# Performance work log

Hardware: AMD Instinct MI355X
Metric: run time of the kernel (lower is better)

## Reference

```python
import jax, jax.numpy as jnp
import numpy as np

DIM = 1024
HEADS = 16
DIM_HEAD = 64
INNER = HEADS * DIM_HEAD
EPS = 1e-5

def layernorm(x, g, b):
    mu = jnp.mean(x, axis=-1, keepdims=True)
    var = jnp.var(x, axis=-1, keepdims=True)
    return (x - mu) * jax.lax.rsqrt(var + EPS) * g + b

def setup_inputs() -> dict:
    key = jax.random.key(0)
    ks = jax.random.split(key, 9)
    b, t, n, m = 8, 8, 576, 64
    x = jax.random.normal(ks[0], (b, t, n, DIM), dtype=jnp.float32)
    latents = jax.random.normal(ks[1], (b, t, m, DIM), dtype=jnp.float32)
    att_mask = jax.random.randint(ks[2], (b, t, n), 0, 2, dtype=jnp.int32)
    s = 1.0 / np.sqrt(DIM)
    Wq = jax.random.normal(ks[3], (DIM, INNER), dtype=jnp.float32) * s
    Wkv = jax.random.normal(ks[4], (DIM, 2 * INNER), dtype=jnp.float32) * s
    Wo = jax.random.normal(ks[5], (INNER, DIM), dtype=jnp.float32) * (1.0 / np.sqrt(INNER))
    gm = jnp.ones((DIM,), jnp.float32); bm = jnp.zeros((DIM,), jnp.float32)
    gl = jnp.ones((DIM,), jnp.float32); bl = jnp.zeros((DIM,), jnp.float32)
    return {"x": x, "latents": latents, "att_mask": att_mask,
            "gm": gm, "bm": bm, "gl": gl, "bl": bl,
            "Wq": Wq, "Wkv": Wkv, "Wo": Wo}

def reference(x, latents, att_mask, gm, bm, gl, bl, Wq, Wkv, Wo):
    b, t, n, d = x.shape
    m = latents.shape[2]
    h, dh = HEADS, DIM_HEAD
    scale = dh ** -0.5

    xn = layernorm(x, gm, bm)
    ln = layernorm(latents, gl, bl)

    q = ln @ Wq                                  # b t m inner
    kv_input = jnp.concatenate((xn, ln), axis=-2)  # b t (n+m) d
    kv = kv_input @ Wkv                          # b t (n+m) 2*inner
    k, v = jnp.split(kv, 2, axis=-1)

    # b t s (h dh) -> b h t s dh
    def split_heads(a):
        bb, tt, ss, _ = a.shape
        return a.reshape(bb, tt, ss, h, dh).transpose(0, 3, 1, 2, 4)
    q = split_heads(q) * scale
    k = split_heads(k)
    v = split_heads(v)

    sim = jnp.einsum('bhtid,bhtjd->bhtij', q, k)   # b h t m (n+m)

    # mask: concat ones for latent KV positions; broadcast over heads and query dim
    full_mask = jnp.concatenate(
        [att_mask.astype(sim.dtype), jnp.ones((b, t, m), sim.dtype)], axis=2)  # b t (n+m)
    neg = jnp.finfo(sim.dtype).min
    bias = jnp.where(full_mask > 0, 0.0, neg)      # b t (n+m)
    sim = sim + bias[:, None, :, None, :]

    attn = jax.nn.softmax(sim, axis=-1)
    out = jnp.einsum('bhtij,bhtjd->bhtid', attn, v)  # b h t m dh
    out = out.transpose(0, 2, 3, 1, 4).reshape(b, t, m, h * dh)
    return out @ Wo
```

## Files before the change

### kernel.cpp

```cpp
#include <hip/hip_runtime.h>
#include <hip/hip_bf16.h>
#include <stdint.h>

#define NCTX 576
#define MLAT 64
#define SEQ 640
#define DMODEL 1024
#define NH 16
#define DHEAD 64
#define INNER_ 1024
#define KV_W 2048

typedef float f32x4 __attribute__((ext_vector_type(4)));
typedef __bf16 bf16x8 __attribute__((ext_vector_type(8)));
typedef unsigned short u16;
typedef unsigned int u32;
typedef unsigned long long u64;

typedef __attribute__((address_space(1))) u32 as1_u32;
typedef __attribute__((address_space(3))) u32 as3_u32;

__device__ __forceinline__ u16 f2bf(float f) {
    u32 u = __builtin_bit_cast(u32, f);
    u32 r = (u + 0x7fffu + ((u >> 16) & 1u)) >> 16;
    return (u16)r;
}

__device__ __forceinline__ int xcd_swizzle(int orig, int nwg) {
    int q = nwg >> 3, r = nwg & 7;
    int xcd = orig & 7, loc = orig >> 3;
    return (xcd < r ? xcd * (q + 1) : r * (q + 1) + (xcd - r) * q) + loc;
}

__global__ __launch_bounds__(256) void transpose_cast(const float* __restrict__ src,
                                                      u16* __restrict__ dst, int K, int N) {
    __shared__ float tile[64][65];
    int k0 = blockIdx.y * 64, n0 = blockIdx.x * 64;
    int tid = threadIdx.x;
#pragma unroll
    for (int i = 0; i < 4; ++i) {
        int idx = i * 256 + tid;
        int kk = idx >> 4;
        int nn = (idx & 15) << 2;
        float4 v = *(const float4*)(src + (u64)(k0 + kk) * N + n0 + nn);
        tile[kk][nn] = v.x; tile[kk][nn + 1] = v.y; tile[kk][nn + 2] = v.z; tile[kk][nn + 3] = v.w;
    }
    __syncthreads();
#pragma unroll
    for (int i = 0; i < 4; ++i) {
        int idx = i * 256 + tid;
        int nn = idx >> 4;
        int kk = (idx & 15) << 2;
        ushort4 o;
        o.x = f2bf(tile[kk][nn]);     o.y = f2bf(tile[kk + 1][nn]);
        o.z = f2bf(tile[kk + 2][nn]); o.w = f2bf(tile[kk + 3][nn]);
        *(ushort4*)(dst + (u64)(n0 + nn) * K + k0 + kk) = o;
    }
}

__global__ __launch_bounds__(256) void ln_cast(const float* __restrict__ x,
                                               const float* __restrict__ lat,
                                               const float* __restrict__ gm, const float* __restrict__ bm,
                                               const float* __restrict__ gl, const float* __restrict__ bl,
                                               u16* __restrict__ out) {
    int row = blockIdx.x;
    int bt = row / SEQ, s = row - bt * SEQ;
    const float *src, *g, *b;
    if (s < NCTX) { src = x + ((u64)bt * NCTX + s) * DMODEL; g = gm; b = bm; }
    else          { src = lat + ((u64)bt * MLAT + (s - NCTX)) * DMODEL; g = gl; b = bl; }
    int tid = threadIdx.x;
    float4 v = *(const float4*)(src + tid * 4);
    float sum = v.x + v.y + v.z + v.w;
    float sq  = v.x * v.x + v.y * v.y + v.z * v.z + v.w * v.w;
#pragma unroll
    for (int off = 1; off < 64; off <<= 1) {
        sum += __shfl_xor(sum, off, 64);
        sq  += __shfl_xor(sq, off, 64);
    }
    __shared__ float red[8];
    int w = tid >> 6, lane = tid & 63;
    if (lane == 0) { red[w] = sum; red[4 + w] = sq; }
    __syncthreads();
    sum = red[0] + red[1] + red[2] + red[3];
    sq  = red[4] + red[5] + red[6] + red[7];
    float mu = sum * (1.0f / DMODEL);
    float var = sq * (1.0f / DMODEL) - mu * mu;
    float rstd = rsqrtf(var + 1e-5f);
    float4 gv = *(const float4*)(g + tid * 4);
    float4 bv = *(const float4*)(b + tid * 4);
    ushort4 o;
    o.x = f2bf((v.x - mu) * rstd * gv.x + bv.x);
    o.y = f2bf((v.y - mu) * rstd * gv.y + bv.y);
    o.z = f2bf((v.z - mu) * rstd * gv.z + bv.z);
    o.w = f2bf((v.w - mu) * rstd * gv.w + bv.w);
    *(ushort4*)(out + (u64)row * DMODEL + tid * 4) = o;
}

template <typename OUT_T>
__global__ __launch_bounds__(256) void gemm_bf16(const u16* __restrict__ A,
                                                 const u16* __restrict__ Bt,
                                                 OUT_T* __restrict__ C,
                                                 int M, int ldc,
                                                 int rpgL2, long long gstride, float scale) {
    constexpr int K = 1024;
    __shared__ u16 As[128 * 32];
    __shared__ u16 Bs[128 * 32];
    int tid = threadIdx.x;
    int lane = tid & 63;
    int w = tid >> 6;
    int wm = w >> 1, wn = w & 1;
    int nwg = gridDim.x * gridDim.y;
    int wg = xcd_swizzle(blockIdx.y * gridDim.x + blockIdx.x, nwg);
    int m0 = (wg / gridDim.x) * 128;
    int n0 = (wg % gridDim.x) * 128;
    u32 rmask = (1u << rpgL2) - 1u;

    f32x4 acc[4][4] = {};

    for (int k0 = 0; k0 < K; k0 += 32) {
        __syncthreads();
#pragma unroll
        for (int i = 0; i < 2; ++i) {
            int t = i * 256 + tid;
            int r = t >> 2;
            int cg = t & 3;
            int col = (cg ^ ((r >> 1) & 3)) << 3;
            int grow = m0 + r; if (grow >= M) grow = M - 1;
            const u16* ga = A + (u64)(grow >> rpgL2) * (u64)gstride + (u64)(grow & rmask) * K + k0 + col;
            __builtin_amdgcn_global_load_lds((const as1_u32*)ga,
                (as3_u32*)(As + ((i * 256 + (w << 6)) << 3)), 16, 0, 0);
            const u16* gb = Bt + (u64)(n0 + r) * K + k0 + col;
            __builtin_amdgcn_global_load_lds((const as1_u32*)gb,
                (as3_u32*)(Bs + ((i * 256 + (w << 6)) << 3)), 16, 0, 0);
        }
        __syncthreads();
        bf16x8 a[4], b[4];
        int rl = lane & 15;
        int cgl = lane >> 4;
#pragma unroll
        for (int mi = 0; mi < 4; ++mi) {
            int r = wm * 64 + mi * 16 + rl;
            int c = (cgl ^ ((r >> 1) & 3)) << 3;
            a[mi] = *(const bf16x8*)(As + r * 32 + c);
        }
#pragma unroll
        for (int ni = 0; ni < 4; ++ni) {
            int r = wn * 64 + ni * 16 + rl;
            int c = (cgl ^ ((r >> 1) & 3)) << 3;
            b[ni] = *(const bf16x8*)(Bs + r * 32 + c);
        }
#pragma unroll
        for (int mi = 0; mi < 4; ++mi)
#pragma unroll
            for (int ni = 0; ni < 4; ++ni)
                acc[mi][ni] = __builtin_amdgcn_mfma_f32_16x16x32_bf16(a[mi], b[ni], acc[mi][ni], 0, 0, 0);
    }
    int rl = lane & 15, rg = lane >> 4;
#pragma unroll
    for (int mi = 0; mi < 4; ++mi) {
#pragma unroll
        for (int r = 0; r < 4; ++r) {
            int grow = m0 + wm * 64 + mi * 16 + rg * 4 + r;
            if (grow < M) {
#pragma unroll
                for (int ni = 0; ni < 4; ++ni) {
                    int gcol = n0 + wn * 64 + ni * 16 + rl;
                    float val = acc[mi][ni][r] * scale;
                    if constexpr (sizeof(OUT_T) == 2)
                        C[(u64)grow * ldc + gcol] = (OUT_T)f2bf(val);
                    else
                        C[(u64)grow * ldc + gcol] = val;
                }
            }
        }
    }
}

__global__ __launch_bounds__(256) void attn_kernel(const u16* __restrict__ qb,
                                                   const u16* __restrict__ kvb,
                                                   const int* __restrict__ mask,
                                                   u16* __restrict__ ob, int bt0) {
    int h = blockIdx.x;
    int btl = blockIdx.y;
    int tid = threadIdx.x, lane = tid & 63, w = tid >> 6;
    __shared__ u16 Ks[64 * 64];
    __shared__ u16 Vt[64 * 64];
    __shared__ u16 Ps[4][16 * 64];
    __shared__ float bias_s[64];

    bf16x8 aq[2];
    {
        int qr = btl * 64 + w * 16 + (lane & 15);
        const u16* qp = qb + (u64)qr * INNER_ + h * 64 + (lane >> 4) * 8;
        aq[0] = *(const bf16x8*)(qp);
        aq[1] = *(const bf16x8*)(qp + 32);
    }
    f32x4 acc[4] = {};
    float mrow[4], lrow[4];
#pragma unroll
    for (int r = 0; r < 4; ++r) { mrow[r] = -1e30f; lrow[r] = 0.f; }

    const u16* kvbase = kvb + (u64)btl * SEQ * KV_W;
    int rl = lane & 15, cgl = lane >> 4;

    for (int c = 0; c < SEQ / 64; ++c) {
        __syncthreads();
#pragma unroll
        for (int i = 0; i < 2; ++i) {
            int t = i * 256 + tid;
            int r = t >> 3;
            int cgp = t & 7;
            int col = (cgp ^ (r & 7)) << 3;
            const u16* gk = kvbase + (u64)(c * 64 + r) * KV_W + h * 64 + col;
            __builtin_amdgcn_global_load_lds((const as1_u32*)gk,
                (as3_u32*)(Ks + ((i * 256 + (w << 6)) << 3)), 16, 0, 0);
        }
#pragma unroll
        for (int i = 0; i < 2; ++i) {
            int t = i * 256 + tid;
            int kvr = t >> 3;
            int d0 = (t & 7) << 3;
            const u16* gv = kvbase + (u64)(c * 64 + kvr) * KV_W + INNER_ + h * 64 + d0;
            ushort4 v0 = *(const ushort4*)gv;
            ushort4 v1 = *(const ushort4*)(gv + 4);
            u16 vals[8] = {v0.x, v0.y, v0.z, v0.w, v1.x, v1.y, v1.z, v1.w};
#pragma unroll
            for (int j = 0; j < 8; ++j) {
                int d = d0 + j;
                int cs = (((kvr >> 3) ^ (d & 7)) << 3) + (kvr & 7);
                Vt[d * 64 + cs] = vals[j];
            }
        }
        if (tid < 64) {
            int pos = c * 64 + tid;
            float bsv = 0.f;
            if (pos < NCTX) bsv = (mask[(bt0 + btl) * NCTX + pos] > 0) ? 0.f : -1e30f;
            bias_s[tid] = bsv;
        }
        __syncthreads();

        f32x4 sf[4];
#pragma unroll
        for (int ni = 0; ni < 4; ++ni) {
            f32x4 z = {};
#pragma unroll
            for (int kk = 0; kk < 2; ++kk) {
                int r = ni * 16 + rl;
                int cc = (((kk * 4 + cgl) ^ (r & 7)) << 3);
                bf16x8 bk = *(const bf16x8*)(Ks + r * 64 + cc);
                z = __builtin_amdgcn_mfma_f32_16x16x32_bf16(aq[kk], bk, z, 0, 0, 0);
            }
            float bias = bias_s[ni * 16 + rl];
            z[0] += bias; z[1] += bias; z[2] += bias; z[3] += bias;
            sf[ni] = z;
        }
        float alpha[4];
#pragma unroll
        for (int r = 0; r < 4; ++r) {
            float m = fmaxf(fmaxf(sf[0][r], sf[1][r]), fmaxf(sf[2][r], sf[3][r]));
            m = fmaxf(m, __shfl_xor(m, 1, 64));
            m = fmaxf(m, __shfl_xor(m, 2, 64));
            m = fmaxf(m, __shfl_xor(m, 4, 64));
            m = fmaxf(m, __shfl_xor(m, 8, 64));
            float mn = fmaxf(mrow[r], m);
            alpha[r] = __expf(mrow[r] - mn);
            mrow[r] = mn;
        }
#pragma unroll
        for (int ni = 0; ni < 4; ++ni)
#pragma unroll
            for (int r = 0; r < 4; ++r)
                sf[ni][r] = __expf(sf[ni][r] - mrow[r]);
#pragma unroll
        for (int r = 0; r < 4; ++r) {
            float s = sf[0][r] + sf[1][r] + sf[2][r] + sf[3][r];
            s += __shfl_xor(s, 1, 64);
            s += __shfl_xor(s, 2, 64);
            s += __shfl_xor(s, 4, 64);
            s += __shfl_xor(s, 8, 64);
            lrow[r] = lrow[r] * alpha[r] + s;
        }
        u16* pw = Ps[w];
#pragma unroll
        for (int ni = 0; ni < 4; ++ni) {
#pragma unroll
            for (int r = 0; r < 4; ++r) {
                int qrow = cgl * 4 + r;
                int kcol = ni * 16 + rl;
                int cs = (((kcol >> 3) ^ (qrow & 7)) << 3) + (kcol & 7);
                pw[qrow * 64 + cs] = f2bf(sf[ni][r]);
            }
        }
#pragma unroll
        for (int oi = 0; oi < 4; ++oi)
#pragma unroll
            for (int r = 0; r < 4; ++r)
                acc[oi][r] *= alpha[r];
        bf16x8 ap[2];
#pragma unroll
        for (int kk = 0; kk < 2; ++kk) {
            int cc = (((kk * 4 + cgl) ^ (rl & 7)) << 3);
            ap[kk] = *(const bf16x8*)(pw + rl * 64 + cc);
        }
#pragma unroll
        for (int oi = 0; oi < 4; ++oi) {
#pragma unroll
            for (int kk = 0; kk < 2; ++kk) {
                int r = oi * 16 + rl;
                int cc = (((kk * 4 + cgl) ^ (r & 7)) << 3);
                bf16x8 bv = *(const bf16x8*)(Vt + r * 64 + cc);
                acc[oi] = __builtin_amdgcn_mfma_f32_16x16x32_bf16(ap[kk], bv, acc[oi], 0, 0, 0);
            }
        }
    }
#pragma unroll
    for (int r = 0; r < 4; ++r) {
        float inv = 1.0f / lrow[r];
        int qrow = btl * 64 + w * 16 + cgl * 4 + r;
        u16* op = ob + (u64)qrow * INNER_ + h * 64;
#pragma unroll
        for (int oi = 0; oi < 4; ++oi)
            op[oi * 16 + rl] = f2bf(acc[oi][r] * inv);
    }
}

extern "C" void kernel_launch(void* const* d_in, const int* in_sizes, int n_in,
                              void* d_out, int out_size, void* d_ws, size_t ws_size,
                              hipStream_t stream) {
    const float* x    = (const float*)d_in[0];
    const float* lat  = (const float*)d_in[1];
    const int*   am   = (const int*)d_in[2];
    const float* gm   = (const float*)d_in[3];
    const float* bm   = (const float*)d_in[4];
    const float* gl   = (const float*)d_in[5];
    const float* bl   = (const float*)d_in[6];
    const float* Wq   = (const float*)d_in[7];
    const float* Wkv  = (const float*)d_in[8];
    const float* Wo   = (const float*)d_in[9];
    float* out = (float*)d_out;

    u16* WqT  = (u16*)d_ws;
    u16* WkvT = WqT + 1024 * 1024;
    u16* WoT  = WkvT + 2048 * 1024;
    u16* bufs = WoT + 1024 * 1024;

    size_t fixed = (size_t)(1024 * 1024 + 2048 * 1024 + 1024 * 1024) * 2;
    size_t perbt = (size_t)(SEQ * DMODEL + SEQ * KV_W + MLAT * DMODEL + MLAT * DMODEL) * 2;
    int C = 64;
    while (C > 1 && fixed + (size_t)C * perbt > ws_size) C >>= 1;

    transpose_cast<<<dim3(16, 16), 256, 0, stream>>>(Wq, WqT, 1024, 1024);
    transpose_cast<<<dim3(32, 16), 256, 0, stream>>>(Wkv, WkvT, 1024, 2048);
    transpose_cast<<<dim3(16, 16), 256, 0, stream>>>(Wo, WoT, 1024, 1024);

    for (int bt0 = 0; bt0 < 64; bt0 += C) {
        u16* xn = bufs;
        u16* kv = xn + (size_t)C * SEQ * DMODEL;
        u16* qb = kv + (size_t)C * SEQ * KV_W;
        u16* ao = qb + (size_t)C * MLAT * DMODEL;

        ln_cast<<<C * SEQ, 256, 0, stream>>>(x + (u64)bt0 * NCTX * DMODEL,
                                             lat + (u64)bt0 * MLAT * DMODEL,
                                             gm, bm, gl, bl, xn);
        gemm_bf16<u16><<<dim3(KV_W / 128, (C * SEQ) / 128), 256, 0, stream>>>(
            xn, WkvT, kv, C * SEQ, KV_W, 30, 0, 1.0f);
        gemm_bf16<u16><<<dim3(INNER_ / 128, (C * MLAT + 127) / 128), 256, 0, stream>>>(
            xn + NCTX * DMODEL, WqT, qb, C * MLAT, INNER_, 6, (long long)SEQ * DMODEL, 0.125f);
        attn_kernel<<<dim3(NH, C), 256, 0, stream>>>(qb, kv, am, ao, bt0);
        gemm_bf16<float><<<dim3(DMODEL / 128, (C * MLAT + 127) / 128), 256, 0, stream>>>(
            ao, WoT, out + (u64)bt0 * MLAT * DMODEL, C * MLAT, DMODEL, 30, 0, 1.0f);
    }
}
```

Measured before the change: 575.9 us.

## Emit V transposed from KV GEMM, double-buffer attention loads, widen GEMM K-tile

The KV projection GEMM now writes V in a transposed per-head layout through a separate epilogue. That lets the attention kernel load both K and V with direct global-to-LDS copies instead of a scalar scatter transpose. The attention kernel also double-buffers K, V and the mask bias so the next chunk's loads overlap compute on the current one. Separately, the GEMM K-step goes from 32 to 64, halving barriers per tile but doubling LDS use. The transposed V stores are strided 8-byte writes, which may cost extra write bandwidth in the GEMM epilogue.

```diff
diff --git a/kernel.cpp b/kernel.cpp
--- a/kernel.cpp
+++ b/kernel.cpp
@@ -7,7 +7,6 @@
 #define SEQ 640
 #define DMODEL 1024
 #define NH 16
-#define DHEAD 64
 #define INNER_ 1024
 #define KV_W 2048
 
@@ -96,15 +95,15 @@
     *(ushort4*)(out + (u64)row * DMODEL + tid * 4) = o;
 }
 
-template <typename OUT_T>
+template <int WRITE_VT, typename OUT_T>
 __global__ __launch_bounds__(256) void gemm_bf16(const u16* __restrict__ A,
                                                  const u16* __restrict__ Bt,
-                                                 OUT_T* __restrict__ C,
+                                                 OUT_T* __restrict__ C, u16* __restrict__ vt,
                                                  int M, int ldc,
                                                  int rpgL2, long long gstride, float scale) {
     constexpr int K = 1024;
-    __shared__ u16 As[128 * 32];
-    __shared__ u16 Bs[128 * 32];
+    __shared__ u16 As[128 * 64];
+    __shared__ u16 Bs[128 * 64];
     int tid = threadIdx.x;
     int lane = tid & 63;
     int w = tid >> 6;
@@ -117,14 +116,14 @@
 
     f32x4 acc[4][4] = {};
 
-    for (int k0 = 0; k0 < K; k0 += 32) {
+    for (int k0 = 0; k0 < K; k0 += 64) {
         __syncthreads();
 #pragma unroll
-        for (int i = 0; i < 2; ++i) {
+        for (int i = 0; i < 4; ++i) {
             int t = i * 256 + tid;
-            int r = t >> 2;
-            int cg = t & 3;
-            int col = (cg ^ ((r >> 1) & 3)) << 3;
+            int r = t >> 3;
+            int cg = t & 7;
+            int col = (cg ^ (r & 7)) << 3;
             int grow = m0 + r; if (grow >= M) grow = M - 1;
             const u16* ga = A + (u64)(grow >> rpgL2) * (u64)gstride + (u64)(grow & rmask) * K + k0 + col;
             __builtin_amdgcn_global_load_lds((const as1_u32*)ga,
@@ -134,42 +133,64 @@
                 (as3_u32*)(Bs + ((i * 256 + (w << 6)) << 3)), 16, 0, 0);
         }
         __syncthreads();
-        bf16x8 a[4], b[4];
-        int rl = lane & 15;
-        int cgl = lane >> 4;
+        int rl = lane & 15, cgl = lane >> 4;
+#pragma unroll
+        for (int kk = 0; kk < 2; ++kk) {
+            bf16x8 a[4], b[4];
+#pragma unroll
+            for (int mi = 0; mi < 4; ++mi) {
+                int r = wm * 64 + mi * 16 + rl;
+                int g = (kk * 4 + cgl) ^ (r & 7);
+                a[mi] = *(const bf16x8*)(As + r * 64 + g * 8);
+            }
+#pragma unroll
+            for (int ni = 0; ni < 4; ++ni) {
+                int r = wn * 64 + ni * 16 + rl;
+                int g = (kk * 4 + cgl) ^ (r & 7);
+                b[ni] = *(const bf16x8*)(Bs + r * 64 + g * 8);
+            }
+#pragma unroll
+            for (int mi = 0; mi < 4; ++mi)
+#pragma unroll
+                for (int ni = 0; ni < 4; ++ni)
+                    acc[mi][ni] = __builtin_amdgcn_mfma_f32_16x16x32_bf16(a[mi], b[ni], acc[mi][ni], 0, 0, 0);
+        }
+    }
+    int rl = lane & 15, rg = lane >> 4;
+    if (WRITE_VT && n0 >= INNER_) {
+        int bt = m0 / SEQ;
+        int s0 = m0 - bt * SEQ + wm * 64;
+#pragma unroll
+        for (int ni = 0; ni < 4; ++ni) {
+            int vcol = (n0 - INNER_) + wn * 64 + ni * 16 + rl;
+            u16* vrow = vt + ((u64)bt * INNER_ + vcol) * SEQ;
+#pragma unroll
+            for (int mi = 0; mi < 4; ++mi) {
+                int s = s0 + mi * 16 + rg * 4;
+                ushort4 o;
+                o.x = f2bf(acc[mi][ni][0] * scale);
+                o.y = f2bf(acc[mi][ni][1] * scale);
+                o.z = f2bf(acc[mi][ni][2] * scale);
+                o.w = f2bf(acc[mi][ni][3] * scale);
+                *(ushort4*)(vrow + s) = o;
+            }
+        }
+    } else {
 #pragma unroll
         for (int mi = 0; mi < 4; ++mi) {
-            int r = wm * 64 + mi * 16 + rl;
-            int c = (cgl ^ ((r >> 1) & 3)) << 3;
-            a[mi] = *(const bf16x8*)(As + r * 32 + c);
-        }
-#pragma unroll
-        for (int ni = 0; ni < 4; ++ni) {
-            int r = wn * 64 + ni * 16 + rl;
-            int c = (cgl ^ ((r >> 1) & 3)) << 3;
-            b[ni] = *(const bf16x8*)(Bs + r * 32 + c);
-        }
-#pragma unroll
-        for (int mi = 0; mi < 4; ++mi)
-#pragma unroll
-            for (int ni = 0; ni < 4; ++ni)
-                acc[mi][ni] = __builtin_amdgcn_mfma_f32_16x16x32_bf16(a[mi], b[ni], acc[mi][ni], 0, 0, 0);
-    }
-    int rl = lane & 15, rg = lane >> 4;
-#pragma unroll
-    for (int mi = 0; mi < 4; ++mi) {
-#pragma unroll
-        for (int r = 0; r < 4; ++r) {
-            int grow = m0 + wm * 64 + mi * 16 + rg * 4 + r;
-            if (grow < M) {
-#pragma unroll
-                for (int ni = 0; ni < 4; ++ni) {
-                    int gcol = n0 + wn * 64 + ni * 16 + rl;
-                    float val = acc[mi][ni][r] * scale;
-                    if constexpr (sizeof(OUT_T) == 2)
-                        C[(u64)grow * ldc + gcol] = (OUT_T)f2bf(val);
-                    else
-                        C[(u64)grow * ldc + gcol] = val;
+#pragma unroll
+            for (int r = 0; r < 4; ++r) {
+                int grow = m0 + wm * 64 + mi * 16 + rg * 4 + r;
+                if (grow < M) {
+#pragma unroll
+                    for (int ni = 0; ni < 4; ++ni) {
+                        int gcol = n0 + wn * 64 + ni * 16 + rl;
+                        float val = acc[mi][ni][r] * scale;
+                        if constexpr (sizeof(OUT_T) == 2)
+                            C[(u64)grow * ldc + gcol] = (OUT_T)f2bf(val);
+                        else
+                            C[(u64)grow * ldc + gcol] = val;
+                    }
                 }
             }
         }
@@ -177,21 +198,23 @@
 }
 
 __global__ __launch_bounds__(256) void attn_kernel(const u16* __restrict__ qb,
-                                                   const u16* __restrict__ kvb,
+                                                   const u16* __restrict__ kbuf,
+                                                   const u16* __restrict__ vtb,
                                                    const int* __restrict__ mask,
                                                    u16* __restrict__ ob, int bt0) {
     int h = blockIdx.x;
     int btl = blockIdx.y;
     int tid = threadIdx.x, lane = tid & 63, w = tid >> 6;
-    __shared__ u16 Ks[64 * 64];
-    __shared__ u16 Vt[64 * 64];
+    __shared__ u16 Ks[2][64 * 64];
+    __shared__ u16 Vs[2][64 * 64];
     __shared__ u16 Ps[4][16 * 64];
-    __shared__ float bias_s[64];
+    __shared__ float bias_s[2][64];
+    int rl = lane & 15, cgl = lane >> 4;
 
     bf16x8 aq[2];
     {
-        int qr = btl * 64 + w * 16 + (lane & 15);
-        const u16* qp = qb + (u64)qr * INNER_ + h * 64 + (lane >> 4) * 8;
+        int qr = btl * MLAT + w * 16 + rl;
+        const u16* qp = qb + (u64)qr * INNER_ + h * 64 + cgl * 8;
         aq[0] = *(const bf16x8*)(qp);
         aq[1] = *(const bf16x8*)(qp + 32);
     }
@@ -200,44 +223,32 @@
 #pragma unroll
     for (int r = 0; r < 4; ++r) { mrow[r] = -1e30f; lrow[r] = 0.f; }
 
-    const u16* kvbase = kvb + (u64)btl * SEQ * KV_W;
-    int rl = lane & 15, cgl = lane >> 4;
-
-    for (int c = 0; c < SEQ / 64; ++c) {
-        __syncthreads();
+    const u16* kbase = kbuf + (u64)btl * SEQ * INNER_ + h * 64;
+    const u16* vbase = vtb + ((u64)btl * INNER_ + h * 64) * SEQ;
+
+    auto stage = [&](int c, int bf) {
 #pragma unroll
         for (int i = 0; i < 2; ++i) {
             int t = i * 256 + tid;
-            int r = t >> 3;
-            int cgp = t & 7;
-            int col = (cgp ^ (r & 7)) << 3;
-            const u16* gk = kvbase + (u64)(c * 64 + r) * KV_W + h * 64 + col;
-            __builtin_amdgcn_global_load_lds((const as1_u32*)gk,
-                (as3_u32*)(Ks + ((i * 256 + (w << 6)) << 3)), 16, 0, 0);
-        }
-#pragma unroll
-        for (int i = 0; i < 2; ++i) {
-            int t = i * 256 + tid;
-            int kvr = t >> 3;
-            int d0 = (t & 7) << 3;
-            const u16* gv = kvbase + (u64)(c * 64 + kvr) * KV_W + INNER_ + h * 64 + d0;
-            ushort4 v0 = *(const ushort4*)gv;
-            ushort4 v1 = *(const ushort4*)(gv + 4);
-            u16 vals[8] = {v0.x, v0.y, v0.z, v0.w, v1.x, v1.y, v1.z, v1.w};
-#pragma unroll
-            for (int j = 0; j < 8; ++j) {
-                int d = d0 + j;
-                int cs = (((kvr >> 3) ^ (d & 7)) << 3) + (kvr & 7);
-                Vt[d * 64 + cs] = vals[j];
-            }
+            int r = t >> 3, cg = t & 7;
+            int col = (cg ^ (r & 7)) << 3;
+            __builtin_amdgcn_global_load_lds((const as1_u32*)(kbase + (u64)(c * 64 + r) * INNER_ + col),
+                (as3_u32*)(&Ks[bf][0] + ((i * 256 + (w << 6)) << 3)), 16, 0, 0);
+            __builtin_amdgcn_global_load_lds((const as1_u32*)(vbase + (u64)r * SEQ + c * 64 + col),
+                (as3_u32*)(&Vs[bf][0] + ((i * 256 + (w << 6)) << 3)), 16, 0, 0);
         }
         if (tid < 64) {
             int pos = c * 64 + tid;
-            float bsv = 0.f;
-            if (pos < NCTX) bsv = (mask[(bt0 + btl) * NCTX + pos] > 0) ? 0.f : -1e30f;
-            bias_s[tid] = bsv;
-        }
-        __syncthreads();
+            bias_s[bf][tid] = (pos < NCTX) ? ((mask[(bt0 + btl) * NCTX + pos] > 0) ? 0.f : -1e30f) : 0.f;
+        }
+    };
+
+    stage(0, 0);
+    __syncthreads();
+
+    for (int c = 0; c < SEQ / 64; ++c) {
+        int bf = c & 1;
+        if (c + 1 < SEQ / 64) stage(c + 1, bf ^ 1);
 
         f32x4 sf[4];
 #pragma unroll
@@ -246,11 +257,11 @@
 #pragma unroll
             for (int kk = 0; kk < 2; ++kk) {
                 int r = ni * 16 + rl;
-                int cc = (((kk * 4 + cgl) ^ (r & 7)) << 3);
-                bf16x8 bk = *(const bf16x8*)(Ks + r * 64 + cc);
+                int g = (kk * 4 + cgl) ^ (r & 7);
+                bf16x8 bk = *(const bf16x8*)(&Ks[bf][0] + r * 64 + g * 8);
                 z = __builtin_amdgcn_mfma_f32_16x16x32_bf16(aq[kk], bk, z, 0, 0, 0);
             }
-            float bias = bias_s[ni * 16 + rl];
+            float bias = bias_s[bf][ni * 16 + rl];
             z[0] += bias; z[1] += bias; z[2] += bias; z[3] += bias;
             sf[ni] = z;
         }
@@ -307,16 +318,17 @@
 #pragma unroll
             for (int kk = 0; kk < 2; ++kk) {
                 int r = oi * 16 + rl;
-                int cc = (((kk * 4 + cgl) ^ (r & 7)) << 3);
-                bf16x8 bv = *(const bf16x8*)(Vt + r * 64 + cc);
+                int g = (kk * 4 + cgl) ^ (r & 7);
+                bf16x8 bv = *(const bf16x8*)(&Vs[bf][0] + r * 64 + g * 8);
                 acc[oi] = __builtin_amdgcn_mfma_f32_16x16x32_bf16(ap[kk], bv, acc[oi], 0, 0, 0);
             }
         }
+        __syncthreads();
     }
 #pragma unroll
     for (int r = 0; r < 4; ++r) {
         float inv = 1.0f / lrow[r];
-        int qrow = btl * 64 + w * 16 + cgl * 4 + r;
+        int qrow = btl * MLAT + w * 16 + cgl * 4 + r;
         u16* op = ob + (u64)qrow * INNER_ + h * 64;
 #pragma unroll
         for (int oi = 0; oi < 4; ++oi)
@@ -345,7 +357,7 @@
     u16* bufs = WoT + 1024 * 1024;
 
     size_t fixed = (size_t)(1024 * 1024 + 2048 * 1024 + 1024 * 1024) * 2;
-    size_t perbt = (size_t)(SEQ * DMODEL + SEQ * KV_W + MLAT * DMODEL + MLAT * DMODEL) * 2;
+    size_t perbt = (size_t)(SEQ * DMODEL + SEQ * INNER_ + INNER_ * SEQ + MLAT * INNER_ + MLAT * INNER_) * 2;
     int C = 64;
     while (C > 1 && fixed + (size_t)C * perbt > ws_size) C >>= 1;
 
@@ -354,20 +366,21 @@
     transpose_cast<<<dim3(16, 16), 256, 0, stream>>>(Wo, WoT, 1024, 1024);
 
     for (int bt0 = 0; bt0 < 64; bt0 += C) {
-        u16* xn = bufs;
-        u16* kv = xn + (size_t)C * SEQ * DMODEL;
-        u16* qb = kv + (size_t)C * SEQ * KV_W;
-        u16* ao = qb + (size_t)C * MLAT * DMODEL;
+        u16* xn  = bufs;
+        u16* kb  = xn + (size_t)C * SEQ * DMODEL;
+        u16* vtp = kb + (size_t)C * SEQ * INNER_;
+        u16* qbp = vtp + (size_t)C * INNER_ * SEQ;
+        u16* ao  = qbp + (size_t)C * MLAT * INNER_;
 
         ln_cast<<<C * SEQ, 256, 0, stream>>>(x + (u64)bt0 * NCTX * DMODEL,
                                              lat + (u64)bt0 * MLAT * DMODEL,
                                              gm, bm, gl, bl, xn);
-        gemm_bf16<u16><<<dim3(KV_W / 128, (C * SEQ) / 128), 256, 0, stream>>>(
-            xn, WkvT, kv, C * SEQ, KV_W, 30, 0, 1.0f);
-        gemm_bf16<u16><<<dim3(INNER_ / 128, (C * MLAT + 127) / 128), 256, 0, stream>>>(
-            xn + NCTX * DMODEL, WqT, qb, C * MLAT, INNER_, 6, (long long)SEQ * DMODEL, 0.125f);
-        attn_kernel<<<dim3(NH, C), 256, 0, stream>>>(qb, kv, am, ao, bt0);
-        gemm_bf16<float><<<dim3(DMODEL / 128, (C * MLAT + 127) / 128), 256, 0, stream>>>(
-            ao, WoT, out + (u64)bt0 * MLAT * DMODEL, C * MLAT, DMODEL, 30, 0, 1.0f);
-    }
-}
+        gemm_bf16<1, u16><<<dim3(KV_W / 128, (C * SEQ) / 128), 256, 0, stream>>>(
+            xn, WkvT, kb, vtp, C * SEQ, INNER_, 30, 0, 1.0f);
+        gemm_bf16<0, u16><<<dim3(INNER_ / 128, (C * MLAT + 127) / 128), 256, 0, stream>>>(
+            xn + NCTX * DMODEL, WqT, qbp, nullptr, C * MLAT, INNER_, 6, (long long)SEQ * DMODEL, 0.125f);
+        attn_kernel<<<dim3(NH, C), 256, 0, stream>>>(qbp, kb, vtp, am, ao, bt0);
+        gemm_bf16<0, float><<<dim3(DMODEL / 128, (C * MLAT + 127) / 128), 256, 0, stream>>>(
+            ao, WoT, out + (u64)bt0 * MLAT * DMODEL, nullptr, C * MLAT, DMODEL, 30, 0, 1.0f);
+    }
+}
```

Measured after the change: 611.7 us. +6.2%, slower.
